# Kernel tuning notes

Hardware: AMD Instinct MI355X
Metric: run time of the kernel (lower is better)

The kernel has to match this reference:

```python
import jax, jax.numpy as jnp
import numpy as np

N_NODES = 50000
N_EDGES = 800000
D_IN, H1, H2, N_CLASSES = 128, 128, 64, 2


def setup_inputs() -> dict:
    key = jax.random.key(0)
    ks = jax.random.split(key, 8)
    x = jax.random.normal(ks[0], (N_NODES, D_IN), dtype=jnp.float32)
    edge_index = jax.random.randint(ks[1], (2, N_EDGES), 0, N_NODES, dtype=jnp.int64)
    s = 1.0 / np.sqrt(D_IN)
    W1 = jax.random.uniform(ks[2], (D_IN, H1), jnp.float32, -s, s)
    b1 = jnp.zeros((H1,), jnp.float32)
    s = 1.0 / np.sqrt(H1)
    W2 = jax.random.uniform(ks[3], (H1, H2), jnp.float32, -s, s)
    b2 = jnp.zeros((H2,), jnp.float32)
    s = 1.0 / np.sqrt(H2)
    Wo = jax.random.uniform(ks[4], (H2, N_CLASSES), jnp.float32, -s, s)
    bo = jax.random.uniform(ks[5], (N_CLASSES,), jnp.float32, -s, s)
    return {"x": x, "edge_index": edge_index, "W1": W1, "b1": b1,
            "W2": W2, "b2": b2, "Wo": Wo, "bo": bo}


def _gcn_conv(x, W, b, src, dst, n_nodes):
    # PyG GCNConv: add self loops, symmetric normalization deg^{-1/2} A deg^{-1/2}
    h = x @ W  # [N, out]
    ones = jnp.ones((src.shape[0],), h.dtype)
    deg = jax.ops.segment_sum(ones, dst, num_segments=n_nodes) + 1.0  # +1 self loop
    dinv = jax.lax.rsqrt(deg)  # deg >= 1 always (self loops)
    coef = dinv[src] * dinv[dst]  # [E]
    msg = h[src] * coef[:, None]  # [E, out] gather
    agg = jax.ops.segment_sum(msg, dst, num_segments=n_nodes)  # scatter-add
    agg = agg + h * (dinv * dinv)[:, None]  # self-loop contribution
    return agg + b


def reference(x, edge_index, W1, b1, W2, b2, Wo, bo):
    src, dst = edge_index[0], edge_index[1]
    n = x.shape[0]
    h = jax.nn.relu(_gcn_conv(x, W1, b1, src, dst, n))
    # dropout p=0.25 is identity in eval mode
    h = jax.nn.relu(_gcn_conv(h, W2, b2, src, dst, n))
    logits = h @ Wo + bo
    return jax.nn.log_softmax(logits, axis=1)
```

## Files before the change

### kernel.cpp

```cpp
#include <hip/hip_runtime.h>
#include <stdint.h>

#define N_NODES 50000
#define N_EDGES 800000
#define CAP 80
#define ZROW N_NODES
#define NBKT 196
#define BKT_CAP 4608
#define NSCAT 256
#define EPB 3125
#define GEMM_BLOCKS 782

typedef __attribute__((ext_vector_type(8))) short short8;
typedef __attribute__((ext_vector_type(4))) float floatx4;

__device__ __forceinline__ float bflo(uint32_t u) { return __uint_as_float(u << 16); }
__device__ __forceinline__ float bfhi(uint32_t u) { return __uint_as_float(u & 0xffff0000u); }
__device__ __forceinline__ unsigned short f2b(float f) {
    uint32_t u = __float_as_uint(f);
    u += 0x7fffu + ((u >> 16) & 1u);
    return (unsigned short)(u >> 16);
}

__global__ __launch_bounds__(256) void k_prep(const float* __restrict__ W1,
                                              const float* __restrict__ W2,
                                              unsigned short* __restrict__ Wt1,
                                              unsigned short* __restrict__ Wt2,
                                              int* __restrict__ gcnt) {
    int gid = blockIdx.x * 256 + threadIdx.x;
    if (gid < 16384) {
        int k = gid >> 7, n = gid & 127;
        Wt1[n * 128 + k] = f2b(W1[gid]);
    } else if (gid < 24576) {
        int j = gid - 16384;
        int k = j >> 6, n = j & 63;
        Wt2[n * 128 + k] = f2b(W2[j]);
    } else if (gid < 24576 + NBKT) {
        gcnt[gid - 24576] = 0;
    }
}

__global__ __launch_bounds__(256) void k_binscat_gemm1(const int* __restrict__ src,
                                                       const int* __restrict__ dst,
                                                       int* __restrict__ gcnt,
                                                       uint32_t* __restrict__ binned,
                                                       const float* __restrict__ x,
                                                       const unsigned short* __restrict__ Wt1,
                                                       unsigned short* __restrict__ h1s,
                                                       unsigned short* __restrict__ h2s) {
    __shared__ unsigned short At[64 * 136];
    __shared__ unsigned short Bt[128 * 136];
    int t = threadIdx.x;
    if (blockIdx.x < NSCAT) {
        int* hist = (int*)At;
        int* cur  = ((int*)At) + 256;
        if (t < NBKT) hist[t] = 0;
        __syncthreads();
        int e0 = blockIdx.x * EPB;
        for (int i = t; i < EPB; i += 256)
            atomicAdd(&hist[dst[e0 + i] >> 8], 1);
        __syncthreads();
        if (t < NBKT) {
            int h = hist[t];
            int off = h ? atomicAdd(&gcnt[t], h) : 0;
            cur[t] = t * BKT_CAP + off;
        }
        __syncthreads();
        for (int i = t; i < EPB; i += 256) {
            int d = dst[e0 + i], s = src[e0 + i];
            int bb = d >> 8;
            int idx = atomicAdd(&cur[bb], 1);
            if (idx < (bb + 1) * BKT_CAP)
                binned[idx] = (uint32_t)s | ((uint32_t)(d & 255) << 16);
        }
        return;
    }
    int row0 = (blockIdx.x - NSCAT) * 64;
    for (int i = t; i < 2048; i += 256) {
        int n = i >> 4, kc = (i & 15) * 8;
        *(uint4*)&Bt[n * 136 + kc] = *(const uint4*)(Wt1 + n * 128 + kc);
    }
    for (int i = t; i < 1024; i += 256) {
        int r = i >> 4, kc = (i & 15) * 8;
        int g = row0 + r; if (g >= N_NODES) g = N_NODES - 1;
        const float* p = x + g * 128 + kc;
        float4 a = *(const float4*)p, b = *(const float4*)(p + 4);
        uint4 o;
        o.x = (uint32_t)f2b(a.x) | ((uint32_t)f2b(a.y) << 16);
        o.y = (uint32_t)f2b(a.z) | ((uint32_t)f2b(a.w) << 16);
        o.z = (uint32_t)f2b(b.x) | ((uint32_t)f2b(b.y) << 16);
        o.w = (uint32_t)f2b(b.z) | ((uint32_t)f2b(b.w) << 16);
        *(uint4*)&At[r * 136 + kc] = o;
    }
    __syncthreads();
    int wv = t >> 6, lane = t & 63;
    int m = lane & 15, qd = lane >> 4;
    floatx4 acc[8];
    #pragma unroll
    for (int c = 0; c < 8; c++) acc[c] = (floatx4){0.f, 0.f, 0.f, 0.f};
    const unsigned short* ap = &At[(wv * 16 + m) * 136 + qd * 8];
    const unsigned short* bp = &Bt[m * 136 + qd * 8];
    #pragma unroll
    for (int kk = 0; kk < 4; kk++) {
        short8 af = *(const short8*)(ap + kk * 32);
        #pragma unroll
        for (int c = 0; c < 8; c++) {
            short8 bf = *(const short8*)(bp + c * 16 * 136 + kk * 32);
            acc[c] = __builtin_amdgcn_mfma_f32_16x16x32_bf16(af, bf, acc[c], 0, 0, 0);
        }
    }
    #pragma unroll
    for (int reg = 0; reg < 4; reg++) {
        int g = row0 + wv * 16 + qd * 4 + reg;
        if (g < N_NODES) {
            #pragma unroll
            for (int c = 0; c < 8; c++)
                h1s[g * 128 + c * 16 + m] = f2b(acc[c][reg]);
        } else {
            #pragma unroll
            for (int c = 0; c < 8; c++)
                h1s[g * 128 + c * 16 + m] = 0;
            #pragma unroll
            for (int c = 0; c < 4; c++)
                h2s[g * 64 + c * 16 + m] = 0;
        }
    }
}

__global__ __launch_bounds__(256) void k_csr(const uint32_t* __restrict__ binned,
                                             const int* __restrict__ gcnt,
                                             unsigned short* __restrict__ csr,
                                             int* __restrict__ counts) {
    __shared__ int cnt[256];
    int t = threadIdx.x, b = blockIdx.x;
    cnt[t] = 0;
    __syncthreads();
    int n = min(gcnt[b], BKT_CAP);
    int node0 = b << 8;
    const uint32_t* w0 = binned + b * BKT_CAP;
    for (int i = t; i < n; i += 256) {
        uint32_t w = w0[i];
        int doff = (int)(w >> 16);
        int r = atomicAdd(&cnt[doff], 1);
        if (r < CAP) csr[(node0 + doff) * CAP + r] = (unsigned short)(w & 0xffffu);
    }
    __syncthreads();
    counts[node0 + t] = cnt[t];
}

__global__ __launch_bounds__(256) void k_agg1g2(const unsigned short* __restrict__ h1s,
                                                const unsigned short* __restrict__ Wt2,
                                                const unsigned short* __restrict__ csr,
                                                const int* __restrict__ counts,
                                                const float* __restrict__ b1,
                                                unsigned short* __restrict__ h2s) {
    __shared__ unsigned short Bt[64 * 136];
    __shared__ unsigned short At[16 * 136];
    int t = threadIdx.x;
    for (int i = t; i < 1024; i += 256) {
        int n = i >> 4, kc = (i & 15) * 8;
        *(uint4*)&Bt[n * 136 + kc] = *(const uint4*)(Wt2 + n * 128 + kc);
    }
    int wv = t >> 6, lane = t & 63;
    int q = lane >> 4, l = lane & 15;
    int v0 = blockIdx.x * 16;
    int v = v0 + wv * 4 + q;
    int n = counts[v];
    float dv = rsqrtf((float)n + 1.0f);
    int n_eff = min(n, CAP);
    const unsigned short* cs = csr + v * CAP;
    int nmax = n_eff;
    nmax = max(nmax, __shfl_xor(nmax, 16));
    nmax = max(nmax, __shfl_xor(nmax, 32));
    float a0, a1, a2, a3, a4, a5, a6, a7;
    {
        uint4 p = *(const uint4*)(h1s + v * 128 + l * 8);
        a0 = dv * bflo(p.x); a1 = dv * bfhi(p.x); a2 = dv * bflo(p.y); a3 = dv * bfhi(p.y);
        a4 = dv * bflo(p.z); a5 = dv * bfhi(p.z); a6 = dv * bflo(p.w); a7 = dv * bfhi(p.w);
    }
    for (int base = 0; base < nmax; base += 16) {
        int idx = base + l;
        int e = (idx < n_eff) ? (int)cs[idx] : ZROW;
        float de = rsqrtf((float)counts[e] + 1.0f);
        int mm = nmax - base; if (mm > 16) mm = 16;
        #pragma unroll 4
        for (int i = 0; i < mm; i++) {
            int s = __shfl(e, (q << 4) + i);
            float di = __shfl(de, (q << 4) + i);
            uint4 p = *(const uint4*)(h1s + s * 128 + l * 8);
            a0 = fmaf(di, bflo(p.x), a0); a1 = fmaf(di, bfhi(p.x), a1);
            a2 = fmaf(di, bflo(p.y), a2); a3 = fmaf(di, bfhi(p.y), a3);
            a4 = fmaf(di, bflo(p.z), a4); a5 = fmaf(di, bfhi(p.z), a5);
            a6 = fmaf(di, bflo(p.w), a6); a7 = fmaf(di, bfhi(p.w), a7);
        }
    }
    {
        float4 bL = *(const float4*)(b1 + l * 8);
        float4 bH = *(const float4*)(b1 + l * 8 + 4);
        a0 = fmaxf(fmaf(dv, a0, bL.x), 0.f); a1 = fmaxf(fmaf(dv, a1, bL.y), 0.f);
        a2 = fmaxf(fmaf(dv, a2, bL.z), 0.f); a3 = fmaxf(fmaf(dv, a3, bL.w), 0.f);
        a4 = fmaxf(fmaf(dv, a4, bH.x), 0.f); a5 = fmaxf(fmaf(dv, a5, bH.y), 0.f);
        a6 = fmaxf(fmaf(dv, a6, bH.z), 0.f); a7 = fmaxf(fmaf(dv, a7, bH.w), 0.f);
        uint4 o;
        o.x = (uint32_t)f2b(a0) | ((uint32_t)f2b(a1) << 16);
        o.y = (uint32_t)f2b(a2) | ((uint32_t)f2b(a3) << 16);
        o.z = (uint32_t)f2b(a4) | ((uint32_t)f2b(a5) << 16);
        o.w = (uint32_t)f2b(a6) | ((uint32_t)f2b(a7) << 16);
        *(uint4*)&At[(wv * 4 + q) * 136 + l * 8] = o;
    }
    __syncthreads();
    int m = lane & 15, qd = lane >> 4;
    floatx4 acc = (floatx4){0.f, 0.f, 0.f, 0.f};
    const unsigned short* ap = &At[m * 136 + qd * 8];
    const unsigned short* bp = &Bt[(wv * 16 + m) * 136 + qd * 8];
    #pragma unroll
    for (int kk = 0; kk < 4; kk++) {
        short8 af = *(const short8*)(ap + kk * 32);
        short8 bf = *(const short8*)(bp + kk * 32);
        acc = __builtin_amdgcn_mfma_f32_16x16x32_bf16(af, bf, acc, 0, 0, 0);
    }
    #pragma unroll
    for (int reg = 0; reg < 4; reg++) {
        int g = v0 + qd * 4 + reg;
        float dg = rsqrtf((float)counts[g] + 1.0f);
        h2s[g * 64 + wv * 16 + m] = f2b(dg * acc[reg]);
    }
}

__global__ __launch_bounds__(256) void k_agg2(const unsigned short* __restrict__ h2s,
                                              const unsigned short* __restrict__ csr,
                                              const int* __restrict__ counts,
                                              const float* __restrict__ b2,
                                              const float* __restrict__ Wo,
                                              const float* __restrict__ bo,
                                              float* __restrict__ out) {
    int wave = (blockIdx.x * 256 + threadIdx.x) >> 6;
    int lane = threadIdx.x & 63;
    int q = lane >> 4, l = lane & 15;
    int h = l >> 3, c = l & 7;
    int v = wave * 4 + q;
    int n = counts[v];
    float dv = rsqrtf((float)n + 1.0f);
    int n_eff = min(n, CAP);
    const unsigned short* cs = csr + v * CAP;
    int nmax = n_eff;
    nmax = max(nmax, __shfl_xor(nmax, 16));
    nmax = max(nmax, __shfl_xor(nmax, 32));
    float a0 = 0.f, a1 = 0.f, a2 = 0.f, a3 = 0.f, a4 = 0.f, a5 = 0.f, a6 = 0.f, a7 = 0.f;
    if (h == 0) {
        uint4 p = *(const uint4*)(h2s + v * 64 + c * 8);
        a0 = bflo(p.x); a1 = bfhi(p.x); a2 = bflo(p.y); a3 = bfhi(p.y);
        a4 = bflo(p.z); a5 = bfhi(p.z); a6 = bflo(p.w); a7 = bfhi(p.w);
    }
    for (int base = 0; base < nmax; base += 16) {
        int idx = base + l;
        int e = (idx < n_eff) ? (int)cs[idx] : ZROW;
        int mm = nmax - base; if (mm > 16) mm = 16;
        int pairs = (mm + 1) >> 1;
        #pragma unroll 4
        for (int i = 0; i < pairs; i++) {
            int s = __shfl(e, (q << 4) + 2 * i + h);
            uint4 p = *(const uint4*)(h2s + s * 64 + c * 8);
            a0 += bflo(p.x); a1 += bfhi(p.x); a2 += bflo(p.y); a3 += bfhi(p.y);
            a4 += bflo(p.z); a5 += bfhi(p.z); a6 += bflo(p.w); a7 += bfhi(p.w);
        }
    }
    a0 += __shfl_xor(a0, 8); a1 += __shfl_xor(a1, 8);
    a2 += __shfl_xor(a2, 8); a3 += __shfl_xor(a3, 8);
    a4 += __shfl_xor(a4, 8); a5 += __shfl_xor(a5, 8);
    a6 += __shfl_xor(a6, 8); a7 += __shfl_xor(a7, 8);
    float4 bL = *(const float4*)(b2 + c * 8);
    float4 bH = *(const float4*)(b2 + c * 8 + 4);
    a0 = fmaxf(fmaf(dv, a0, bL.x), 0.f); a1 = fmaxf(fmaf(dv, a1, bL.y), 0.f);
    a2 = fmaxf(fmaf(dv, a2, bL.z), 0.f); a3 = fmaxf(fmaf(dv, a3, bL.w), 0.f);
    a4 = fmaxf(fmaf(dv, a4, bH.x), 0.f); a5 = fmaxf(fmaf(dv, a5, bH.y), 0.f);
    a6 = fmaxf(fmaf(dv, a6, bH.z), 0.f); a7 = fmaxf(fmaf(dv, a7, bH.w), 0.f);
    float4 wA = *(const float4*)(Wo + c * 16);
    float4 wB = *(const float4*)(Wo + c * 16 + 4);
    float4 wC = *(const float4*)(Wo + c * 16 + 8);
    float4 wD = *(const float4*)(Wo + c * 16 + 12);
    float l0 = a0 * wA.x + a1 * wA.z + a2 * wB.x + a3 * wB.z
             + a4 * wC.x + a5 * wC.z + a6 * wD.x + a7 * wD.z;
    float l1 = a0 * wA.y + a1 * wA.w + a2 * wB.y + a3 * wB.w
             + a4 * wC.y + a5 * wC.w + a6 * wD.y + a7 * wD.w;
    l0 += __shfl_xor(l0, 1); l1 += __shfl_xor(l1, 1);
    l0 += __shfl_xor(l0, 2); l1 += __shfl_xor(l1, 2);
    l0 += __shfl_xor(l0, 4); l1 += __shfl_xor(l1, 4);
    if (l == 0) {
        float2 bof = *(const float2*)bo;
        l0 += bof.x; l1 += bof.y;
        float m = fmaxf(l0, l1);
        float ls = m + __logf(__expf(l0 - m) + __expf(l1 - m));
        *(float2*)(out + v * 2) = make_float2(l0 - ls, l1 - ls);
    }
}

extern "C" void kernel_launch(void* const* d_in, const int* in_sizes, int n_in,
                              void* d_out, int out_size, void* d_ws, size_t ws_size,
                              hipStream_t stream) {
    const float* x  = (const float*)d_in[0];
    const int* ei   = (const int*)d_in[1];
    const float* W1 = (const float*)d_in[2];
    const float* b1 = (const float*)d_in[3];
    const float* W2 = (const float*)d_in[4];
    const float* b2 = (const float*)d_in[5];
    const float* Wo = (const float*)d_in[6];
    const float* bo = (const float*)d_in[7];
    float* out      = (float*)d_out;
    const int* src = ei;
    const int* dst = ei + N_EDGES;

    char* w = (char*)d_ws;
    int* counts = (int*)(w + 0);
    unsigned short* csr = (unsigned short*)(w + 200704);
    unsigned short* Wt1 = (unsigned short*)(w + 8228864);
    unsigned short* Wt2 = (unsigned short*)(w + 8261632);
    unsigned short* h1s = (unsigned short*)(w + 8278016);
    unsigned short* h2s = (unsigned short*)(w + 21090304);
    uint32_t* binned = (uint32_t*)(w + 27496448);
    int* gcnt = (int*)(w + 31109120);

    k_prep         <<<97, 256, 0, stream>>>(W1, W2, Wt1, Wt2, gcnt);
    k_binscat_gemm1<<<NSCAT + GEMM_BLOCKS, 256, 0, stream>>>(src, dst, gcnt, binned,
                                                             x, Wt1, h1s, h2s);
    k_csr          <<<NBKT, 256, 0, stream>>>(binned, gcnt, csr, counts);
    k_agg1g2       <<<3125, 256, 0, stream>>>(h1s, Wt2, csr, counts, b1, h2s);
    k_agg2         <<<3125, 256, 0, stream>>>(h2s, csr, counts, b2, Wo, bo, out);
}
```

Measured before the change: 166.6 us.

## Prescale h1 rows by source degree norm and vectorize edge binning loads

The CSR kernel now also computes each node's deg^-1/2 and multiplies the bf16 h1 rows by it in place. The first aggregation can then sum neighbour rows with plain adds, with no per-edge counts lookup, rsqrt or shuffle. The binning pass reads src/dst as int4 vectors with 250 blocks of 800 vectors each. The cost is an extra read-modify-write of h1 in the CSR kernel and a second bf16 rounding of the scaled values. Rows past N_NODES in the last bucket are also touched, assuming h1s has padding.

```diff
diff --git a/kernel.cpp b/kernel.cpp
--- a/kernel.cpp
+++ b/kernel.cpp
@@ -7,8 +7,8 @@
 #define ZROW N_NODES
 #define NBKT 196
 #define BKT_CAP 4608
-#define NSCAT 256
-#define EPB 3125
+#define NSCAT 250
+#define EPB4 800
 #define GEMM_BLOCKS 782
 
 typedef __attribute__((ext_vector_type(8))) short short8;
@@ -56,9 +56,15 @@
         int* cur  = ((int*)At) + 256;
         if (t < NBKT) hist[t] = 0;
         __syncthreads();
-        int e0 = blockIdx.x * EPB;
-        for (int i = t; i < EPB; i += 256)
-            atomicAdd(&hist[dst[e0 + i] >> 8], 1);
+        const int4* d4 = (const int4*)dst + blockIdx.x * EPB4;
+        const int4* s4 = (const int4*)src + blockIdx.x * EPB4;
+        for (int j = t; j < EPB4; j += 256) {
+            int4 dv = d4[j];
+            atomicAdd(&hist[dv.x >> 8], 1);
+            atomicAdd(&hist[dv.y >> 8], 1);
+            atomicAdd(&hist[dv.z >> 8], 1);
+            atomicAdd(&hist[dv.w >> 8], 1);
+        }
         __syncthreads();
         if (t < NBKT) {
             int h = hist[t];
@@ -66,12 +72,15 @@
             cur[t] = t * BKT_CAP + off;
         }
         __syncthreads();
-        for (int i = t; i < EPB; i += 256) {
-            int d = dst[e0 + i], s = src[e0 + i];
-            int bb = d >> 8;
-            int idx = atomicAdd(&cur[bb], 1);
-            if (idx < (bb + 1) * BKT_CAP)
-                binned[idx] = (uint32_t)s | ((uint32_t)(d & 255) << 16);
+        for (int j = t; j < EPB4; j += 256) {
+            int4 dv = d4[j];
+            int4 sv = s4[j];
+#define SCAT1(dd, ss) { int bb = (dd) >> 8;                                          \
+            int idx = atomicAdd(&cur[bb], 1);                                        \
+            if (idx < (bb + 1) * BKT_CAP)                                            \
+                binned[idx] = (uint32_t)(ss) | ((uint32_t)((dd) & 255) << 16); }
+            SCAT1(dv.x, sv.x) SCAT1(dv.y, sv.y) SCAT1(dv.z, sv.z) SCAT1(dv.w, sv.w)
+#undef SCAT1
         }
         return;
     }
@@ -127,11 +136,13 @@
     }
 }
 
-__global__ __launch_bounds__(256) void k_csr(const uint32_t* __restrict__ binned,
-                                             const int* __restrict__ gcnt,
-                                             unsigned short* __restrict__ csr,
-                                             int* __restrict__ counts) {
+__global__ __launch_bounds__(256) void k_csr_scale(const uint32_t* __restrict__ binned,
+                                                   const int* __restrict__ gcnt,
+                                                   unsigned short* __restrict__ csr,
+                                                   int* __restrict__ counts,
+                                                   unsigned short* __restrict__ h1s) {
     __shared__ int cnt[256];
+    __shared__ float dis[256];
     int t = threadIdx.x, b = blockIdx.x;
     cnt[t] = 0;
     __syncthreads();
@@ -145,7 +156,22 @@
         if (r < CAP) csr[(node0 + doff) * CAP + r] = (unsigned short)(w & 0xffffu);
     }
     __syncthreads();
-    counts[node0 + t] = cnt[t];
+    int deg = cnt[t];
+    counts[node0 + t] = deg;
+    dis[t] = rsqrtf((float)deg + 1.0f);
+    __syncthreads();
+    for (int i = t; i < 4096; i += 256) {
+        int r = i >> 4, kc = (i & 15) * 8;
+        float di = dis[r];
+        unsigned short* p = h1s + (node0 + r) * 128 + kc;
+        uint4 v = *(const uint4*)p;
+        uint4 o;
+        o.x = (uint32_t)f2b(di * bflo(v.x)) | ((uint32_t)f2b(di * bfhi(v.x)) << 16);
+        o.y = (uint32_t)f2b(di * bflo(v.y)) | ((uint32_t)f2b(di * bfhi(v.y)) << 16);
+        o.z = (uint32_t)f2b(di * bflo(v.z)) | ((uint32_t)f2b(di * bfhi(v.z)) << 16);
+        o.w = (uint32_t)f2b(di * bflo(v.w)) | ((uint32_t)f2b(di * bfhi(v.w)) << 16);
+        *(uint4*)p = o;
+    }
 }
 
 __global__ __launch_bounds__(256) void k_agg1g2(const unsigned short* __restrict__ h1s,
@@ -175,23 +201,19 @@
     float a0, a1, a2, a3, a4, a5, a6, a7;
     {
         uint4 p = *(const uint4*)(h1s + v * 128 + l * 8);
-        a0 = dv * bflo(p.x); a1 = dv * bfhi(p.x); a2 = dv * bflo(p.y); a3 = dv * bfhi(p.y);
-        a4 = dv * bflo(p.z); a5 = dv * bfhi(p.z); a6 = dv * bflo(p.w); a7 = dv * bfhi(p.w);
+        a0 = bflo(p.x); a1 = bfhi(p.x); a2 = bflo(p.y); a3 = bfhi(p.y);
+        a4 = bflo(p.z); a5 = bfhi(p.z); a6 = bflo(p.w); a7 = bfhi(p.w);
     }
     for (int base = 0; base < nmax; base += 16) {
         int idx = base + l;
         int e = (idx < n_eff) ? (int)cs[idx] : ZROW;
-        float de = rsqrtf((float)counts[e] + 1.0f);
         int mm = nmax - base; if (mm > 16) mm = 16;
         #pragma unroll 4
         for (int i = 0; i < mm; i++) {
             int s = __shfl(e, (q << 4) + i);
-            float di = __shfl(de, (q << 4) + i);
             uint4 p = *(const uint4*)(h1s + s * 128 + l * 8);
-            a0 = fmaf(di, bflo(p.x), a0); a1 = fmaf(di, bfhi(p.x), a1);
-            a2 = fmaf(di, bflo(p.y), a2); a3 = fmaf(di, bfhi(p.y), a3);
-            a4 = fmaf(di, bflo(p.z), a4); a5 = fmaf(di, bfhi(p.z), a5);
-            a6 = fmaf(di, bflo(p.w), a6); a7 = fmaf(di, bfhi(p.w), a7);
+            a0 += bflo(p.x); a1 += bfhi(p.x); a2 += bflo(p.y); a3 += bfhi(p.y);
+            a4 += bflo(p.z); a5 += bfhi(p.z); a6 += bflo(p.w); a7 += bfhi(p.w);
         }
     }
     {
@@ -323,7 +345,7 @@
     k_prep         <<<97, 256, 0, stream>>>(W1, W2, Wt1, Wt2, gcnt);
     k_binscat_gemm1<<<NSCAT + GEMM_BLOCKS, 256, 0, stream>>>(src, dst, gcnt, binned,
                                                              x, Wt1, h1s, h2s);
-    k_csr          <<<NBKT, 256, 0, stream>>>(binned, gcnt, csr, counts);
+    k_csr_scale    <<<NBKT, 256, 0, stream>>>(binned, gcnt, csr, counts, h1s);
     k_agg1g2       <<<3125, 256, 0, stream>>>(h1s, Wt2, csr, counts, b1, h2s);
     k_agg2         <<<3125, 256, 0, stream>>>(h2s, csr, counts, b2, Wo, bo, out);
 }
```

Measured after the change: 169.5 us. No clear change (+1.8%).
